# Performance work log

Hardware: AMD Instinct MI355X
Metric: run time of the kernel (lower is better)

## Reference

```python
import jax, jax.numpy as jnp
import numpy as np

N = 100000        # nodes
E = 3200000       # directed edges (already includes both directions per the repo)
F_IN = 256
HID = 16
C = 40


def setup_inputs() -> dict:
    key = jax.random.key(0)
    k = jax.random.split(key, 5)
    x = jax.random.normal(k[0], (N, F_IN), dtype=jnp.float32)
    edge_index = jax.random.randint(k[1], (2, E), 0, N, dtype=jnp.int64)
    W1 = jax.random.normal(k[2], (F_IN, HID), dtype=jnp.float32) * (1.0 / np.sqrt(F_IN))
    b1 = jnp.zeros((HID,), jnp.float32)
    W2 = jax.random.normal(k[3], (HID, C), dtype=jnp.float32) * (1.0 / np.sqrt(HID))
    b2 = jnp.zeros((C,), jnp.float32)
    return {"x": x, "edge_index": edge_index, "W1": W1, "b1": b1, "W2": W2, "b2": b2}


def reference(x, edge_index, W1, b1, W2, b2):
    n = x.shape[0]
    # GCNConv: add self-loops, symmetric degree normalization (shared by both layers)
    loop = jnp.arange(n, dtype=edge_index.dtype)
    src = jnp.concatenate([edge_index[0], loop])
    dst = jnp.concatenate([edge_index[1], loop])
    deg = jax.ops.segment_sum(jnp.ones_like(dst, x.dtype), dst, num_segments=n)
    dinv = jnp.where(deg > 0, jax.lax.rsqrt(deg), 0.0)
    norm = dinv[src] * dinv[dst]  # [E+N]

    def gcn(h, W, b):
        h = h @ W  # transform first (PyG order), keeps edge messages low-dim
        msg = h[src] * norm[:, None]
        return jax.ops.segment_sum(msg, dst, num_segments=n) + b

    h = jax.nn.relu(gcn(x, W1, b1))
    # dropout is identity in eval mode (training=False)
    logits = gcn(h, W2, b2)
    return jax.nn.log_softmax(logits, axis=1)
```

## Files before the change

### kernel.cpp

```cpp
#include <hip/hip_runtime.h>
#include <hip/hip_bf16.h>


#define BSH 8
#define BCAP 9216
#define MAXB 512
#define OVF_CAP 8192
#define EPB 4096

typedef __attribute__((ext_vector_type(8))) short bf16x8;
typedef __attribute__((ext_vector_type(4))) float f32x4;

__device__ __forceinline__ short f2b(float f) {
    __hip_bfloat16 h = __float2bfloat16(f);
    return *reinterpret_cast<short*>(&h);
}
__device__ __forceinline__ float b2f(short s) {
    return __uint_as_float(((unsigned int)(unsigned short)s) << 16);
}

__global__ __launch_bounds__(512) void binA(
        const int* __restrict__ src, const int* __restrict__ dst,
        int* __restrict__ gcur, int* __restrict__ padded,
        int2* __restrict__ ovf, int* __restrict__ ovf_cnt,
        int* __restrict__ deg, int E) {
    __shared__ int hist[MAXB], gb[MAXB];
    int tid = threadIdx.x;
    int e0 = blockIdx.x * EPB;
    int e1 = min(e0 + EPB, E);
    if (tid < MAXB) hist[tid] = 0;
    __syncthreads();
    int rs[8], rd[8];
#pragma unroll
    for (int u = 0; u < 8; ++u) {
        int i = e0 + tid + u * 512;
        if (i < e1) {
            rd[u] = dst[i];
            rs[u] = src[i];
            atomicAdd(&hist[rd[u] >> BSH], 1);
        }
    }
    __syncthreads();
    if (tid < MAXB) {
        int h = hist[tid];
        gb[tid] = h ? atomicAdd(&gcur[tid], h) : 0;
        hist[tid] = 0;
    }
    __syncthreads();
#pragma unroll
    for (int u = 0; u < 8; ++u) {
        int i = e0 + tid + u * 512;
        if (i < e1) {
            int s = rs[u], d = rd[u];
            int b = d >> BSH;
            int r = atomicAdd(&hist[b], 1);
            int off = gb[b] + r;
            if (off < BCAP) {
                padded[b * BCAP + off] = (s << BSH) | (d & ((1 << BSH) - 1));
            } else {
                int k = atomicAdd(ovf_cnt, 1);
                if (k < OVF_CAP) ovf[k] = make_int2(s, d);
                atomicAdd(&deg[d], 1);
            }
        }
    }
}

__global__ __launch_bounds__(1024) void binB(
        const int* __restrict__ gcur, int* __restrict__ padded,
        int2* __restrict__ og, int* __restrict__ deg, int n) {
    __shared__ int bins[256], scanb[256], sA[256];
    __shared__ int sorted[BCAP];
    int k = blockIdx.x, tid = threadIdx.x;
    int base = k * BCAP;
    int cnt = gcur[k];
    if (cnt > BCAP) cnt = BCAP;
    if (cnt < 0) cnt = 0;
    if (tid < 256) bins[tid] = 0;
    __syncthreads();
    for (int i = tid; i < cnt; i += 1024)
        atomicAdd(&bins[padded[base + i] & 255], 1);
    __syncthreads();
    if (tid < 256) sA[tid] = bins[tid];
    __syncthreads();
    for (int d = 1; d < 256; d <<= 1) {
        int v = 0, a = 0;
        if (tid < 256) {
            v = sA[tid];
            a = (tid >= d) ? sA[tid - d] : 0;
        }
        __syncthreads();
        if (tid < 256) sA[tid] = v + a;
        __syncthreads();
    }
    if (tid < 256) {
        int excl = sA[tid] - bins[tid];
        scanb[tid] = excl;
        int node = (k << BSH) + tid;
        if (node < n) {
            og[node] = make_int2(base + excl, bins[tid]);
            atomicAdd(&deg[node], bins[tid]);
        }
        bins[tid] = 0;
    }
    __syncthreads();
    for (int i = tid; i < cnt; i += 1024) {
        int v = padded[base + i];
        int lo = v & 255;
        int r = atomicAdd(&bins[lo], 1);
        sorted[scanb[lo] + r] = v >> BSH;
    }
    __syncthreads();
    for (int i = tid; i < cnt; i += 1024) padded[base + i] = sorted[i];
}

__global__ __launch_bounds__(512) void gemm1_mfma(
        const float* __restrict__ x, const float* __restrict__ W1,
        const int* __restrict__ deg, float* __restrict__ dinv,
        short* __restrict__ t1b, int n) {
    __shared__ __align__(16) short xs[128 * 264];
    __shared__ short w1s[256 * 16];
    int tid = threadIdx.x;
    int base = blockIdx.x * 128;
    int rows = n - base; if (rows > 128) rows = 128;

    for (int i = tid; i < 4096; i += 512) w1s[i] = f2b(W1[i]);
    for (int i = tid; i < 8192; i += 512) {
        int r = i >> 6, c = i & 63;
        if (r < rows) {
            float4 v = ((const float4*)(x + (size_t)(base + r) * 256))[c];
            short4 b;
            b.x = f2b(v.x); b.y = f2b(v.y); b.z = f2b(v.z); b.w = f2b(v.w);
            *(short4*)&xs[r * 264 + c * 4] = b;
        }
    }
    __syncthreads();

    int lane = tid & 63, wave = tid >> 6;
    int q = lane >> 4, m = lane & 15;

    bf16x8 bfrag[8];
#pragma unroll
    for (int t = 0; t < 8; ++t)
#pragma unroll
        for (int j = 0; j < 8; ++j)
            bfrag[t][j] = w1s[(t * 32 + q * 8 + j) * 16 + m];

    f32x4 acc = {0.f, 0.f, 0.f, 0.f};
    int arow = wave * 16 + m;
#pragma unroll
    for (int t = 0; t < 8; ++t) {
        bf16x8 a = *(const bf16x8*)&xs[arow * 264 + t * 32 + q * 8];
        acc = __builtin_amdgcn_mfma_f32_16x16x32_bf16(a, bfrag[t], acc, 0, 0, 0);
    }
#pragma unroll
    for (int r = 0; r < 4; ++r) {
        int node = base + wave * 16 + q * 4 + r;
        if (node < n) {
            float di = rsqrtf((float)deg[node] + 1.0f);
            t1b[(size_t)node * 16 + m] = f2b(acc[r] * di);
            if (m == 0) dinv[node] = di;
        }
    }
}

template <int PHASE>
__global__ __launch_bounds__(256) void agg_k(
        const int2* __restrict__ og, const int* __restrict__ padded,
        const short* __restrict__ feat, float* __restrict__ Sout,
        short* __restrict__ Hout, const float* __restrict__ dinv,
        const float* __restrict__ b1, int n) {
    int node = blockIdx.x * 128 + (threadIdx.x >> 1);
    int q    = threadIdx.x & 1;
    if (node >= n) return;
    const bf16x8* f8 = (const bf16x8*)feat;
    float acc[8];
    bf16x8 sv = f8[(size_t)node * 2 + q];
#pragma unroll
    for (int h = 0; h < 8; ++h) acc[h] = b2f(sv[h]);
    int2 o = og[node];
    int b = o.x, c = o.y, j = 0;
    for (; j + 4 <= c; j += 4) {
        int s0 = padded[b + j],     s1 = padded[b + j + 1];
        int s2 = padded[b + j + 2], s3 = padded[b + j + 3];
        bf16x8 v0 = f8[(size_t)s0 * 2 + q];
        bf16x8 v1 = f8[(size_t)s1 * 2 + q];
        bf16x8 v2 = f8[(size_t)s2 * 2 + q];
        bf16x8 v3 = f8[(size_t)s3 * 2 + q];
#pragma unroll
        for (int h = 0; h < 8; ++h)
            acc[h] += (b2f(v0[h]) + b2f(v1[h])) + (b2f(v2[h]) + b2f(v3[h]));
    }
    for (; j < c; ++j) {
        bf16x8 v = f8[(size_t)padded[b + j] * 2 + q];
#pragma unroll
        for (int h = 0; h < 8; ++h) acc[h] += b2f(v[h]);
    }
    if (PHASE == 0) {
        float di = dinv[node];
        const float4* b4 = (const float4*)b1;
        float4 bA = b4[q * 2], bB = b4[q * 2 + 1];
        bf16x8 o8;
        o8[0] = f2b(fmaxf(bA.x + di * acc[0], 0.f) * di);
        o8[1] = f2b(fmaxf(bA.y + di * acc[1], 0.f) * di);
        o8[2] = f2b(fmaxf(bA.z + di * acc[2], 0.f) * di);
        o8[3] = f2b(fmaxf(bA.w + di * acc[3], 0.f) * di);
        o8[4] = f2b(fmaxf(bB.x + di * acc[4], 0.f) * di);
        o8[5] = f2b(fmaxf(bB.y + di * acc[5], 0.f) * di);
        o8[6] = f2b(fmaxf(bB.z + di * acc[6], 0.f) * di);
        o8[7] = f2b(fmaxf(bB.w + di * acc[7], 0.f) * di);
        ((bf16x8*)(Hout + (size_t)node * 16))[q] = o8;
    } else {
        float4* o4 = (float4*)(Sout + (size_t)node * 16 + q * 8);
        o4[0] = make_float4(acc[0], acc[1], acc[2], acc[3]);
        o4[1] = make_float4(acc[4], acc[5], acc[6], acc[7]);
    }
}

__global__ __launch_bounds__(256) void final_k(
        const float* __restrict__ S2, const float* __restrict__ dinv,
        const float* __restrict__ W2, const float* __restrict__ b2,
        float* __restrict__ out, int n) {
    __shared__ float W2s[16 * 40];
    __shared__ float b2s[40];
    for (int i = threadIdx.x; i < 640; i += 256) W2s[i] = W2[i];
    if (threadIdx.x < 40) b2s[threadIdx.x] = b2[threadIdx.x];
    __syncthreads();
    int node = blockIdx.x * blockDim.x + threadIdx.x;
    if (node >= n) return;
    float di = dinv[node];
    float g[16];
    const float4* a4 = (const float4*)(S2 + (size_t)node * 16);
    float4 t0 = a4[0], t1 = a4[1], t2 = a4[2], t3 = a4[3];
    g[0]=di*t0.x; g[1]=di*t0.y; g[2]=di*t0.z; g[3]=di*t0.w;
    g[4]=di*t1.x; g[5]=di*t1.y; g[6]=di*t1.z; g[7]=di*t1.w;
    g[8]=di*t2.x; g[9]=di*t2.y; g[10]=di*t2.z; g[11]=di*t2.w;
    g[12]=di*t3.x; g[13]=di*t3.y; g[14]=di*t3.z; g[15]=di*t3.w;
    float lg[40];
    float mx = -1e30f;
#pragma unroll
    for (int j = 0; j < 40; ++j) {
        float acc = b2s[j];
#pragma unroll
        for (int k = 0; k < 16; ++k) acc += g[k] * W2s[k * 40 + j];
        lg[j] = acc;
        mx = fmaxf(mx, acc);
    }
    float sum = 0.f;
#pragma unroll
    for (int j = 0; j < 40; ++j) sum += __expf(lg[j] - mx);
    float lse = mx + logf(sum);
    float4* o4 = (float4*)(out + (size_t)node * 40);
#pragma unroll
    for (int j = 0; j < 10; ++j) {
        float4 v;
        v.x = lg[4 * j + 0] - lse;
        v.y = lg[4 * j + 1] - lse;
        v.z = lg[4 * j + 2] - lse;
        v.w = lg[4 * j + 3] - lse;
        o4[j] = v;
    }
}

extern "C" void kernel_launch(void* const* d_in, const int* in_sizes, int n_in,
                              void* d_out, int out_size, void* d_ws, size_t ws_size,
                              hipStream_t stream) {
    const float* x  = (const float*)d_in[0];
    const int*   ei = (const int*)d_in[1];
    const float* W1 = (const float*)d_in[2];
    const float* b1 = (const float*)d_in[3];
    const float* W2 = (const float*)d_in[4];
    const float* b2 = (const float*)d_in[5];

    int n = in_sizes[0] / 256;
    int E = in_sizes[1] / 2;
    const int* srcp = ei;
    const int* dstp = ei + E;

    int nbuckets = (n + 255) >> BSH;

    int2*  og      = (int2*)d_ws;
    int*   deg     = (int*)d_ws + 2 * (size_t)n;
    int*   gcur    = deg + n;
    int*   ovf_cnt = gcur + MAXB;
    float* dinv    = (float*)(ovf_cnt + 16);
    int2*  ovf     = (int2*)(dinv + n);
    short* t1b     = (short*)(ovf + OVF_CAP);
    short* hdb     = t1b + 16 * (size_t)n;
    float* Sbuf    = (float*)(hdb + 16 * (size_t)n);
    int*   padded  = (int*)(Sbuf + 16 * (size_t)n);
    float* out     = (float*)d_out;

    int gb_n = (n + 255) / 256;

    hipMemsetAsync(deg, 0, (size_t)(n + MAXB + 16) * sizeof(int), stream);
    binA      <<<(E + EPB - 1) / EPB, 512, 0, stream>>>(srcp, dstp, gcur, padded,
                                                        ovf, ovf_cnt, deg, E);
    binB      <<<nbuckets, 1024, 0, stream>>>(gcur, padded, og, deg, n);
    gemm1_mfma<<<(n + 127) / 128, 512, 0, stream>>>(x, W1, deg, dinv, t1b, n);
    agg_k<0>  <<<(n + 127) / 128, 256, 0, stream>>>(og, padded, t1b, nullptr,
                                                    hdb, dinv, b1, n);
    agg_k<1>  <<<(n + 127) / 128, 256, 0, stream>>>(og, padded, hdb, Sbuf,
                                                    nullptr, nullptr, nullptr, n);
    final_k   <<<gb_n, 256, 0, stream>>>(Sbuf, dinv, W2, b2, out, n);
}
```

Baseline: 314.0 us.

## Fuse final projection and log-softmax into layer-2 aggregation; split nodes across four lanes

```diff
diff --git a/kernel.cpp b/kernel.cpp
--- a/kernel.cpp
+++ b/kernel.cpp
@@ -9,6 +9,7 @@
 #define EPB 4096
 
 typedef __attribute__((ext_vector_type(8))) short bf16x8;
+typedef __attribute__((ext_vector_type(4))) short bf16x4;
 typedef __attribute__((ext_vector_type(4))) float f32x4;
 
 __device__ __forceinline__ short f2b(float f) {
@@ -167,98 +168,95 @@
 template <int PHASE>
 __global__ __launch_bounds__(256) void agg_k(
         const int2* __restrict__ og, const int* __restrict__ padded,
-        const short* __restrict__ feat, float* __restrict__ Sout,
+        const short* __restrict__ feat,
         short* __restrict__ Hout, const float* __restrict__ dinv,
-        const float* __restrict__ b1, int n) {
-    int node = blockIdx.x * 128 + (threadIdx.x >> 1);
-    int q    = threadIdx.x & 1;
-    if (node >= n) return;
-    const bf16x8* f8 = (const bf16x8*)feat;
-    float acc[8];
-    bf16x8 sv = f8[(size_t)node * 2 + q];
-#pragma unroll
-    for (int h = 0; h < 8; ++h) acc[h] = b2f(sv[h]);
-    int2 o = og[node];
-    int b = o.x, c = o.y, j = 0;
+        const float* __restrict__ b1,
+        const float* __restrict__ W2, const float* __restrict__ b2,
+        float* __restrict__ out, int n) {
+    __shared__ float W2s[640];
+    __shared__ float b2s[40];
+    __shared__ float sAcc[64][17];
+    int tid = threadIdx.x;
+    if (PHASE == 1) {
+        for (int i = tid; i < 640; i += 256) W2s[i] = W2[i];
+        if (tid < 40) b2s[tid] = b2[tid];
+        __syncthreads();
+    }
+    int nl   = tid >> 2;
+    int node = blockIdx.x * 64 + nl;
+    int q    = tid & 3;
+    bool live = node < n;
+    const bf16x4* f4 = (const bf16x4*)feat;
+    float acc[4] = {0.f, 0.f, 0.f, 0.f};
+    int b = 0, c = 0;
+    if (live) {
+        bf16x4 sv = f4[(size_t)node * 4 + q];
+        acc[0] = b2f(sv[0]); acc[1] = b2f(sv[1]);
+        acc[2] = b2f(sv[2]); acc[3] = b2f(sv[3]);
+        int2 o = og[node]; b = o.x; c = o.y;
+    }
+    int j = 0;
     for (; j + 4 <= c; j += 4) {
         int s0 = padded[b + j],     s1 = padded[b + j + 1];
         int s2 = padded[b + j + 2], s3 = padded[b + j + 3];
-        bf16x8 v0 = f8[(size_t)s0 * 2 + q];
-        bf16x8 v1 = f8[(size_t)s1 * 2 + q];
-        bf16x8 v2 = f8[(size_t)s2 * 2 + q];
-        bf16x8 v3 = f8[(size_t)s3 * 2 + q];
-#pragma unroll
-        for (int h = 0; h < 8; ++h)
+        bf16x4 v0 = f4[(size_t)s0 * 4 + q];
+        bf16x4 v1 = f4[(size_t)s1 * 4 + q];
+        bf16x4 v2 = f4[(size_t)s2 * 4 + q];
+        bf16x4 v3 = f4[(size_t)s3 * 4 + q];
+#pragma unroll
+        for (int h = 0; h < 4; ++h)
             acc[h] += (b2f(v0[h]) + b2f(v1[h])) + (b2f(v2[h]) + b2f(v3[h]));
     }
     for (; j < c; ++j) {
-        bf16x8 v = f8[(size_t)padded[b + j] * 2 + q];
-#pragma unroll
-        for (int h = 0; h < 8; ++h) acc[h] += b2f(v[h]);
-    }
+        bf16x4 v = f4[(size_t)padded[b + j] * 4 + q];
+#pragma unroll
+        for (int h = 0; h < 4; ++h) acc[h] += b2f(v[h]);
+    }
+
     if (PHASE == 0) {
-        float di = dinv[node];
-        const float4* b4 = (const float4*)b1;
-        float4 bA = b4[q * 2], bB = b4[q * 2 + 1];
-        bf16x8 o8;
-        o8[0] = f2b(fmaxf(bA.x + di * acc[0], 0.f) * di);
-        o8[1] = f2b(fmaxf(bA.y + di * acc[1], 0.f) * di);
-        o8[2] = f2b(fmaxf(bA.z + di * acc[2], 0.f) * di);
-        o8[3] = f2b(fmaxf(bA.w + di * acc[3], 0.f) * di);
-        o8[4] = f2b(fmaxf(bB.x + di * acc[4], 0.f) * di);
-        o8[5] = f2b(fmaxf(bB.y + di * acc[5], 0.f) * di);
-        o8[6] = f2b(fmaxf(bB.z + di * acc[6], 0.f) * di);
-        o8[7] = f2b(fmaxf(bB.w + di * acc[7], 0.f) * di);
-        ((bf16x8*)(Hout + (size_t)node * 16))[q] = o8;
+        if (live) {
+            float di = dinv[node];
+            float4 bb = ((const float4*)b1)[q];
+            bf16x4 o4_;
+            o4_[0] = f2b(fmaxf(bb.x + di * acc[0], 0.f) * di);
+            o4_[1] = f2b(fmaxf(bb.y + di * acc[1], 0.f) * di);
+            o4_[2] = f2b(fmaxf(bb.z + di * acc[2], 0.f) * di);
+            o4_[3] = f2b(fmaxf(bb.w + di * acc[3], 0.f) * di);
+            ((bf16x4*)Hout)[(size_t)node * 4 + q] = o4_;
+        }
     } else {
-        float4* o4 = (float4*)(Sout + (size_t)node * 16 + q * 8);
-        o4[0] = make_float4(acc[0], acc[1], acc[2], acc[3]);
-        o4[1] = make_float4(acc[4], acc[5], acc[6], acc[7]);
-    }
-}
-
-__global__ __launch_bounds__(256) void final_k(
-        const float* __restrict__ S2, const float* __restrict__ dinv,
-        const float* __restrict__ W2, const float* __restrict__ b2,
-        float* __restrict__ out, int n) {
-    __shared__ float W2s[16 * 40];
-    __shared__ float b2s[40];
-    for (int i = threadIdx.x; i < 640; i += 256) W2s[i] = W2[i];
-    if (threadIdx.x < 40) b2s[threadIdx.x] = b2[threadIdx.x];
-    __syncthreads();
-    int node = blockIdx.x * blockDim.x + threadIdx.x;
-    if (node >= n) return;
-    float di = dinv[node];
-    float g[16];
-    const float4* a4 = (const float4*)(S2 + (size_t)node * 16);
-    float4 t0 = a4[0], t1 = a4[1], t2 = a4[2], t3 = a4[3];
-    g[0]=di*t0.x; g[1]=di*t0.y; g[2]=di*t0.z; g[3]=di*t0.w;
-    g[4]=di*t1.x; g[5]=di*t1.y; g[6]=di*t1.z; g[7]=di*t1.w;
-    g[8]=di*t2.x; g[9]=di*t2.y; g[10]=di*t2.z; g[11]=di*t2.w;
-    g[12]=di*t3.x; g[13]=di*t3.y; g[14]=di*t3.z; g[15]=di*t3.w;
-    float lg[40];
-    float mx = -1e30f;
-#pragma unroll
-    for (int j = 0; j < 40; ++j) {
-        float acc = b2s[j];
-#pragma unroll
-        for (int k = 0; k < 16; ++k) acc += g[k] * W2s[k * 40 + j];
-        lg[j] = acc;
-        mx = fmaxf(mx, acc);
-    }
-    float sum = 0.f;
-#pragma unroll
-    for (int j = 0; j < 40; ++j) sum += __expf(lg[j] - mx);
-    float lse = mx + logf(sum);
-    float4* o4 = (float4*)(out + (size_t)node * 40);
-#pragma unroll
-    for (int j = 0; j < 10; ++j) {
-        float4 v;
-        v.x = lg[4 * j + 0] - lse;
-        v.y = lg[4 * j + 1] - lse;
-        v.z = lg[4 * j + 2] - lse;
-        v.w = lg[4 * j + 3] - lse;
-        o4[j] = v;
+        float di = live ? dinv[node] : 0.f;
+#pragma unroll
+        for (int h = 0; h < 4; ++h) sAcc[nl][q * 4 + h] = di * acc[h];
+        __syncthreads();
+        float gf[16];
+#pragma unroll
+        for (int k = 0; k < 16; ++k) gf[k] = sAcc[nl][k];
+        float lg[10];
+        float mx = -1e30f;
+#pragma unroll
+        for (int jj = 0; jj < 10; ++jj) {
+            int col = q * 10 + jj;
+            float a = b2s[col];
+#pragma unroll
+            for (int k = 0; k < 16; ++k) a += gf[k] * W2s[k * 40 + col];
+            lg[jj] = a;
+            mx = fmaxf(mx, a);
+        }
+        mx = fmaxf(mx, __shfl_xor(mx, 1));
+        mx = fmaxf(mx, __shfl_xor(mx, 2));
+        float sum = 0.f;
+#pragma unroll
+        for (int jj = 0; jj < 10; ++jj) sum += __expf(lg[jj] - mx);
+        sum += __shfl_xor(sum, 1);
+        sum += __shfl_xor(sum, 2);
+        float lse = mx + logf(sum);
+        if (live) {
+            float2* o2 = (float2*)(out + (size_t)node * 40 + q * 10);
+#pragma unroll
+            for (int jj = 0; jj < 5; ++jj)
+                o2[jj] = make_float2(lg[2 * jj] - lse, lg[2 * jj + 1] - lse);
+        }
     }
 }
 
@@ -287,20 +285,17 @@
     int2*  ovf     = (int2*)(dinv + n);
     short* t1b     = (short*)(ovf + OVF_CAP);
     short* hdb     = t1b + 16 * (size_t)n;
-    float* Sbuf    = (float*)(hdb + 16 * (size_t)n);
-    int*   padded  = (int*)(Sbuf + 16 * (size_t)n);
+    int*   padded  = (int*)(hdb + 16 * (size_t)n);
     float* out     = (float*)d_out;
-
-    int gb_n = (n + 255) / 256;
 
     hipMemsetAsync(deg, 0, (size_t)(n + MAXB + 16) * sizeof(int), stream);
     binA      <<<(E + EPB - 1) / EPB, 512, 0, stream>>>(srcp, dstp, gcur, padded,
                                                         ovf, ovf_cnt, deg, E);
     binB      <<<nbuckets, 1024, 0, stream>>>(gcur, padded, og, deg, n);
     gemm1_mfma<<<(n + 127) / 128, 512, 0, stream>>>(x, W1, deg, dinv, t1b, n);
-    agg_k<0>  <<<(n + 127) / 128, 256, 0, stream>>>(og, padded, t1b, nullptr,
-                                                    hdb, dinv, b1, n);
-    agg_k<1>  <<<(n + 127) / 128, 256, 0, stream>>>(og, padded, hdb, Sbuf,
-                                                    nullptr, nullptr, nullptr, n);
-    final_k   <<<gb_n, 256, 0, stream>>>(Sbuf, dinv, W2, b2, out, n);
-}
+    agg_k<0>  <<<(n + 63) / 64, 256, 0, stream>>>(og, padded, t1b, hdb, dinv,
+                                                  b1, nullptr, nullptr, nullptr, n);
+    agg_k<1>  <<<(n + 63) / 64, 256, 0, stream>>>(og, padded, hdb, nullptr, dinv,
+                                                  nullptr, W2, b2, out, n);
+    final_dummy:;
+}
```

Result: faster. 301.0 us (-4.1%).
